# Kernel tuning notes

Hardware: AMD Instinct MI355X
Metric: run time of the kernel (lower is better)

The kernel has to match this reference:

```python
import jax, jax.numpy as jnp
import numpy as np

N = 50000
NUM_GRAPHS = 64
EPS = 1e-16  # PyG softmax denominator epsilon


def _gat_conv(x, src, dst, W, a_src, a_dst, b, heads, out_ch):
    n = x.shape[0]
    h = (x @ W).reshape(n, heads, out_ch)                    # [N,H,C]
    al_s = jnp.einsum('nhc,hc->nh', h, a_src)                # [N,H]
    al_d = jnp.einsum('nhc,hc->nh', h, a_dst)                # [N,H]
    e = jax.nn.leaky_relu(al_s[src] + al_d[dst], 0.2)        # [E,H]
    emax = jax.ops.segment_max(e, dst, num_segments=n)       # [N,H]
    ee = jnp.exp(e - emax[dst])
    den = jax.ops.segment_sum(ee, dst, num_segments=n)       # [N,H]
    alpha = ee / (den[dst] + EPS)                            # [E,H]
    msg = h[src] * alpha[:, :, None]                         # [E,H,C]
    out = jax.ops.segment_sum(msg, dst, num_segments=n)      # [N,H,C]
    return out.reshape(n, heads * out_ch) + b


def setup_inputs() -> dict:
    key = jax.random.key(0)
    ks = jax.random.split(key, 16)
    E = 250000
    x = jax.random.normal(ks[0], (N, 11), dtype=jnp.float32)
    edge_index = jax.random.randint(ks[1], (2, E), 0, N, dtype=jnp.int64)
    batch = jnp.sort(jax.random.randint(ks[2], (N,), 0, NUM_GRAPHS, dtype=jnp.int64))
    def glorot(k, shape):
        fan = shape[0] + shape[-1]
        return jax.random.uniform(k, shape, jnp.float32, -1.0, 1.0) * np.sqrt(6.0 / fan)
    return {
        'x': x, 'edge_index': edge_index, 'batch': batch,
        'W1': glorot(ks[3], (11, 8 * 128)),
        'a1s': glorot(ks[4], (8, 128)), 'a1d': glorot(ks[5], (8, 128)),
        'b1': jnp.zeros((8 * 128,), jnp.float32),
        'W2': glorot(ks[6], (1024, 8 * 64)),
        'a2s': glorot(ks[7], (8, 64)), 'a2d': glorot(ks[8], (8, 64)),
        'b2': jnp.zeros((8 * 64,), jnp.float32),
        'W3': glorot(ks[9], (512, 4 * 32)),
        'a3s': glorot(ks[10], (4, 32)), 'a3d': glorot(ks[11], (4, 32)),
        'b3': jnp.zeros((4 * 32,), jnp.float32),
        'Wout': glorot(ks[12], (128, 1)),
        'bout': jnp.zeros((1,), jnp.float32),
    }


def reference(x, edge_index, batch, W1, a1s, a1d, b1, W2, a2s, a2d, b2,
              W3, a3s, a3d, b3, Wout, bout):
    n = x.shape[0]
    # GATConv adds self-loops by default
    loop = jnp.arange(n, dtype=edge_index.dtype)
    src = jnp.concatenate([edge_index[0], loop])
    dst = jnp.concatenate([edge_index[1], loop])
    h = jax.nn.leaky_relu(_gat_conv(x, src, dst, W1, a1s, a1d, b1, 8, 128), 0.01)
    h = jax.nn.leaky_relu(_gat_conv(h, src, dst, W2, a2s, a2d, b2, 8, 64), 0.01)
    h = jax.nn.leaky_relu(_gat_conv(h, src, dst, W3, a3s, a3d, b3, 4, 32), 0.01)
    # global mean pool over graphs
    sums = jax.ops.segment_sum(h, batch, num_segments=NUM_GRAPHS)      # [G,128]
    cnt = jax.ops.segment_sum(jnp.ones((n,), h.dtype), batch, num_segments=NUM_GRAPHS)
    pooled = sums / jnp.maximum(cnt, 1.0)[:, None]
    return pooled @ Wout + bout                                        # [G,1]
```

## Files before the change

kernel.cpp:

```cpp
#include <hip/hip_runtime.h>

#define EPS 1e-16f

typedef __attribute__((ext_vector_type(8))) short short8;
typedef __attribute__((ext_vector_type(4))) float f32x4;

__device__ __forceinline__ float b2f(unsigned short u) {
    return __uint_as_float(((unsigned)u) << 16);
}
__device__ __forceinline__ unsigned short f2b(float f) {
    unsigned u = __float_as_uint(f);
    u += 0x7fffu + ((u >> 16) & 1u);
    return (unsigned short)(u >> 16);
}

typedef __attribute__((address_space(3))) void lds_vp;
typedef __attribute__((address_space(1))) const void glb_vp;
__device__ __forceinline__ void load_lds16(const unsigned short* g,
                                           unsigned short* l) {
    __builtin_amdgcn_global_load_lds((glb_vp*)g, (lds_vp*)l, 16, 0, 0);
}

__global__ void init_deg_kernel(int* deg, int N) {
    int i = blockIdx.x * blockDim.x + threadIdx.x;
    if (i < N) deg[i] = 1;
}

__global__ void hist_kernel(const int* __restrict__ ei, int E, int N, int* deg) {
    int e = blockIdx.x * blockDim.x + threadIdx.x;
    if (e < E) {
        int d = ei[E + e];
        if ((unsigned)d < (unsigned)N) atomicAdd(&deg[d], 1);
    }
}

__global__ void scan_block_kernel(const int* __restrict__ deg,
                                  int* __restrict__ rowst,
                                  int* __restrict__ bsum, int N) {
    __shared__ int s[256];
    int t = threadIdx.x, b = blockIdx.x;
    int i = b * 256 + t;
    s[t] = (i < N) ? deg[i] : 0;
    __syncthreads();
    for (int o = 1; o < 256; o <<= 1) {
        int a = (t >= o) ? s[t - o] : 0;
        __syncthreads();
        s[t] += a;
        __syncthreads();
    }
    if (i < N) rowst[i + 1] = s[t];
    if (t == 255) bsum[b] = s[255];
}

__global__ void scan_top_kernel(const int* __restrict__ bsum,
                                int* __restrict__ boff, int NB) {
    __shared__ int psum[65];
    int t = threadIdx.x;
    int chunk = (NB + 63) / 64;
    int lo = t * chunk, hi = lo + chunk;
    if (lo > NB) lo = NB;
    if (hi > NB) hi = NB;
    int s = 0;
    for (int i = lo; i < hi; i++) s += bsum[i];
    psum[t + 1] = s;
    __syncthreads();
    if (t == 0) {
        psum[0] = 0;
        for (int i = 1; i <= 64; i++) psum[i] += psum[i - 1];
    }
    __syncthreads();
    int run = psum[t];
    for (int i = lo; i < hi; i++) {
        boff[i] = run;
        run += bsum[i];
    }
}

__global__ void scan_add_kernel(int* __restrict__ rowst,
                                const int* __restrict__ boff, int N) {
    int i = blockIdx.x * 256 + threadIdx.x;
    if (i == 0) rowst[0] = 0;
    if (i < N) rowst[i + 1] += boff[blockIdx.x];
}

__global__ void selfloop_kernel(const int* __restrict__ rowst, int* srcs,
                                int* cursor, int N) {
    int n = blockIdx.x * blockDim.x + threadIdx.x;
    if (n < N) {
        srcs[rowst[n]] = n;
        cursor[n] = rowst[n] + 1;
    }
}

__global__ void scatter_kernel(const int* __restrict__ ei, int E, int N,
                               int* cursor, int* srcs) {
    int e = blockIdx.x * blockDim.x + threadIdx.x;
    if (e < E) {
        int d = ei[E + e];
        if ((unsigned)d < (unsigned)N) {
            int p = atomicAdd(&cursor[d], 1);
            int s = ei[e];
            if ((unsigned)s >= (unsigned)N) s = d;
            srcs[p] = s;
        }
    }
}

__global__ void wa1_kernel(const float* __restrict__ W1,
                           const float* __restrict__ a1s,
                           const float* __restrict__ a1d,
                           float* __restrict__ w_as, float* __restrict__ w_ad) {
    int t = threadIdx.x;
    if (t >= 88) return;
    int h = t / 11, k = t % 11;
    float s = 0.f, d = 0.f;
    for (int c = 0; c < 128; c++) {
        float w = W1[k * 1024 + h * 128 + c];
        s += w * a1s[h * 128 + c];
        d += w * a1d[h * 128 + c];
    }
    w_as[h * 16 + k] = s;
    w_ad[h * 16 + k] = d;
}

__global__ void al1_kernel(const float* __restrict__ x,
                           const float* __restrict__ w_as,
                           const float* __restrict__ w_ad,
                           float* __restrict__ als, float* __restrict__ ald,
                           int N) {
    int i = blockIdx.x * blockDim.x + threadIdx.x;
    if (i >= N * 8) return;
    int n = i >> 3, h = i & 7;
    float s = 0.f, d = 0.f;
#pragma unroll
    for (int k = 0; k < 11; k++) {
        float xv = x[n * 11 + k];
        s += xv * w_as[h * 16 + k];
        d += xv * w_ad[h * 16 + k];
    }
    als[i] = s;
    ald[i] = d;
}

__global__ void aggx_kernel(const float* __restrict__ x,
                            const float* __restrict__ escr,
                            const int* __restrict__ rowst,
                            const int* __restrict__ srcs,
                            unsigned short* __restrict__ A2, int N) {
    int n = blockIdx.x;
    int t = threadIdx.x;
    int h = t >> 4, k = t & 15;
    int start = rowst[n], end = rowst[n + 1];
    float acc = 0.f;
    const int CH = 4;
    for (int idx = start; idx < end; idx += CH) {
        int mc = end - idx;
        if (mc > CH) mc = CH;
        int ss[CH];
        float av[CH], xv[CH];
#pragma unroll
        for (int j = 0; j < CH; j++)
            if (j < mc) ss[j] = srcs[idx + j];
#pragma unroll
        for (int j = 0; j < CH; j++)
            if (j < mc) av[j] = escr[(size_t)(idx + j) * 8 + h];
#pragma unroll
        for (int j = 0; j < CH; j++)
            if (j < mc) xv[j] = (k < 11) ? x[ss[j] * 11 + k] : 0.f;
#pragma unroll
        for (int j = 0; j < CH; j++)
            if (j < mc) acc += av[j] * xv[j];
    }
    A2[(size_t)n * 128 + t] = f2b(acc);
}

__global__ void w1bd_kernel(const float* __restrict__ W1,
                            unsigned short* __restrict__ Bt) {
    int i = blockIdx.x * blockDim.x + threadIdx.x;
    if (i >= 1024 * 128) return;
    int n = i >> 7, kk = i & 127;
    int h = kk >> 4, k = kk & 15;
    float v = (h == (n >> 7) && k < 11) ? W1[k * 1024 + n] : 0.f;
    Bt[i] = f2b(v);
}

__global__ void transpose_w_kernel(const float* __restrict__ W,
                                   unsigned short* __restrict__ Wt, int K, int N) {
    int i = blockIdx.x * blockDim.x + threadIdx.x;
    if (i >= K * N) return;
    int k = i / N, n = i % N;
    Wt[(size_t)n * K + k] = f2b(W[i]);
}

template <bool EPI, int HB, int CC>
__global__ __launch_bounds__(256) void gemm_mfma(
    const unsigned short* __restrict__ A, const unsigned short* __restrict__ Bt,
    unsigned short* __restrict__ C, const float* __restrict__ bias,
    const float* __restrict__ a_s, const float* __restrict__ a_d,
    float* __restrict__ als, float* __restrict__ ald, int H, int M, int N,
    int K) {
    int NX = gridDim.x;
    int bid = blockIdx.y * NX + blockIdx.x;
    int win = bid & (8 * NX - 1);
    int mg = bid / (8 * NX);
    int m_t = mg * 8 + (win & 7);
    int n_t = win >> 3;
    int bm = m_t * 128, bn = n_t * 128;
    if (bm >= M) return;

    union SMem {
        struct {
            unsigned short As[2][128 * 32];
            unsigned short Bs[2][128 * 32];
        } k;
        unsigned short Ct[128 * 132];
    };
    __shared__ __align__(16) SMem sm;
    auto& As = sm.k.As;
    auto& Bs = sm.k.Bs;
    auto& Ct = sm.Ct;

    int t = threadIdx.x;
    int w = t >> 6, lane = t & 63;
    int quad = lane >> 4, l16 = lane & 15;
    int wr = (w >> 1) * 64, wc = (w & 1) * 64;

    int c0 = w * 128 + lane;
    int c1 = c0 + 64;
    int r0 = c0 >> 2, p0 = c0 & 3;
    int r1 = c1 >> 2, p1 = c1 & 3;
    int j0 = (p0 - (r0 >> 1)) & 3;
    int j1 = (p1 - (r1 >> 1)) & 3;
    int ga0 = bm + r0;
    if (ga0 >= M) ga0 = M - 1;
    int ga1 = bm + r1;
    if (ga1 >= M) ga1 = M - 1;
    const unsigned short* Ag0 = A + (size_t)ga0 * K + j0 * 8;
    const unsigned short* Ag1 = A + (size_t)ga1 * K + j1 * 8;
    const unsigned short* Bg0 = Bt + (size_t)(bn + r0) * K + j0 * 8;
    const unsigned short* Bg1 = Bt + (size_t)(bn + r1) * K + j1 * 8;

    auto stage = [&](int st, int k0) {
        load_lds16(Ag0 + k0, &As[st][(w * 128) * 8]);
        load_lds16(Ag1 + k0, &As[st][(w * 128 + 64) * 8]);
        load_lds16(Bg0 + k0, &Bs[st][(w * 128) * 8]);
        load_lds16(Bg1 + k0, &Bs[st][(w * 128 + 64) * 8]);
    };

    int aoff[4], boff4[4];
#pragma unroll
    for (int i = 0; i < 4; i++) {
        int ra = wr + i * 16 + l16;
        aoff[i] = ra * 32 + (((quad + (ra >> 1)) & 3) * 8);
        int rb = wc + i * 16 + l16;
        boff4[i] = rb * 32 + (((quad + (rb >> 1)) & 3) * 8);
    }

    f32x4 acc[4][4] = {};
    stage(0, 0);
    int st = 0;
    for (int k0 = 0; k0 < K; k0 += 32, st ^= 1) {
        __syncthreads();
        if (k0 + 32 < K) stage(st ^ 1, k0 + 32);
        short8 a[4], b[4];
#pragma unroll
        for (int mi = 0; mi < 4; mi++) a[mi] = *(const short8*)&As[st][aoff[mi]];
#pragma unroll
        for (int ni = 0; ni < 4; ni++) b[ni] = *(const short8*)&Bs[st][boff4[ni]];
#pragma unroll
        for (int mi = 0; mi < 4; mi++)
#pragma unroll
            for (int ni = 0; ni < 4; ni++)
                acc[mi][ni] = __builtin_amdgcn_mfma_f32_16x16x32_bf16(
                    a[mi], b[ni], acc[mi][ni], 0, 0, 0);
    }
    __syncthreads();

#pragma unroll
    for (int mi = 0; mi < 4; mi++) {
#pragma unroll
        for (int r = 0; r < 4; r++) {
            int rl = wr + mi * 16 + quad * 4 + r;
#pragma unroll
            for (int ni = 0; ni < 4; ni++) {
                int cl = wc + ni * 16 + l16;
                float v = acc[mi][ni][r];
                if (EPI) {
                    v += bias[bn + cl];
                    v = v > 0.f ? v : 0.01f * v;
                }
                Ct[rl * 132 + cl] = f2b(v);
            }
        }
    }
    __syncthreads();
#pragma unroll
    for (int p = 0; p < 16; p++) {
        int q = p * 256 + t;
        int row = q >> 5, c8 = q & 31;
        if (bm + row < M) {
            uint2 v = *(const uint2*)&Ct[row * 132 + c8 * 4];
            *(uint2*)&C[(size_t)(bm + row) * N + bn + c8 * 4] = v;
        }
    }
    if (HB > 0) {
        for (int pi = t; pi < 128 * HB; pi += 256) {
            int row = pi / HB, hl = pi % HB;
            if (bm + row >= M) continue;
            int hg = bn / CC + hl;
            const unsigned short* rp = &Ct[row * 132 + hl * CC];
            const float* asp = a_s + hg * CC;
            const float* adp = a_d + hg * CC;
            float s = 0.f, d = 0.f;
#pragma unroll
            for (int c = 0; c < CC; c++) {
                float v = b2f(rp[c]);
                s += v * asp[c];
                d += v * adp[c];
            }
            als[(size_t)(bm + row) * H + hg] = s;
            ald[(size_t)(bm + row) * H + hg] = d;
        }
    }
}

template <int H>
__global__ void mden_kernel(const float* __restrict__ als,
                            const float* __restrict__ ald,
                            const int* __restrict__ rowst,
                            const int* __restrict__ srcs,
                            float* __restrict__ escr, int N) {
    int i = blockIdx.x * blockDim.x + threadIdx.x;
    if (i >= N * H) return;
    int n = i / H, h = i % H;
    float aldn = ald[i];
    int start = rowst[n], end = rowst[n + 1];
    const int CH = 4;
    float m = -1e30f;
    for (int idx = start; idx < end; idx += CH) {
        int mc = end - idx;
        if (mc > CH) mc = CH;
        int ss[CH];
        float lv[CH];
#pragma unroll
        for (int j = 0; j < CH; j++)
            if (j < mc) ss[j] = srcs[idx + j];
#pragma unroll
        for (int j = 0; j < CH; j++)
            if (j < mc) lv[j] = als[ss[j] * H + h];
#pragma unroll
        for (int j = 0; j < CH; j++)
            if (j < mc) {
                float v = lv[j] + aldn;
                v = v > 0.f ? v : 0.2f * v;
                m = fmaxf(m, v);
            }
    }
    float den = 0.f;
    for (int idx = start; idx < end; idx += CH) {
        int mc = end - idx;
        if (mc > CH) mc = CH;
        int ss[CH];
        float lv[CH];
#pragma unroll
        for (int j = 0; j < CH; j++)
            if (j < mc) ss[j] = srcs[idx + j];
#pragma unroll
        for (int j = 0; j < CH; j++)
            if (j < mc) lv[j] = als[ss[j] * H + h];
#pragma unroll
        for (int j = 0; j < CH; j++)
            if (j < mc) {
                float v = lv[j] + aldn;
                v = v > 0.f ? v : 0.2f * v;
                den += expf(v - m);
            }
    }
    float dinv = 1.0f / (den + EPS);
    for (int idx = start; idx < end; idx += CH) {
        int mc = end - idx;
        if (mc > CH) mc = CH;
        int ss[CH];
        float lv[CH];
#pragma unroll
        for (int j = 0; j < CH; j++)
            if (j < mc) ss[j] = srcs[idx + j];
#pragma unroll
        for (int j = 0; j < CH; j++)
            if (j < mc) lv[j] = als[ss[j] * H + h];
#pragma unroll
        for (int j = 0; j < CH; j++)
            if (j < mc) {
                float v = lv[j] + aldn;
                v = v > 0.f ? v : 0.2f * v;
                escr[(size_t)(idx + j) * H + h] = expf(v - m) * dinv;
            }
    }
}

template <int H, int C>
__global__ void agg_kernel4(const unsigned short* __restrict__ hin,
                            const float* __restrict__ escr,
                            const int* __restrict__ rowst,
                            const int* __restrict__ srcs,
                            const float* __restrict__ bias,
                            unsigned short* __restrict__ out, int N) {
    constexpr int HC = H * C;
    int n = blockIdx.x;
    int t = threadIdx.x;
    int c = t * 4;
    int hh = c / C;
    int start = rowst[n], end = rowst[n + 1];
    float a0 = 0.f, a1 = 0.f, a2 = 0.f, a3 = 0.f;
    const int CH = 4;
    for (int idx = start; idx < end; idx += CH) {
        int mc = end - idx;
        if (mc > CH) mc = CH;
        int ss[CH];
        float av[CH];
        ushort4 uv[CH];
#pragma unroll
        for (int j = 0; j < CH; j++)
            if (j < mc) ss[j] = srcs[idx + j];
#pragma unroll
        for (int j = 0; j < CH; j++)
            if (j < mc) av[j] = escr[(size_t)(idx + j) * H + hh];
#pragma unroll
        for (int j = 0; j < CH; j++)
            if (j < mc) uv[j] = *(const ushort4*)(hin + (size_t)ss[j] * HC + c);
#pragma unroll
        for (int j = 0; j < CH; j++)
            if (j < mc) {
                a0 += av[j] * b2f(uv[j].x);
                a1 += av[j] * b2f(uv[j].y);
                a2 += av[j] * b2f(uv[j].z);
                a3 += av[j] * b2f(uv[j].w);
            }
    }
    float v0 = a0 + bias[c], v1 = a1 + bias[c + 1];
    float v2 = a2 + bias[c + 2], v3 = a3 + bias[c + 3];
    ushort4 o;
    o.x = f2b(v0 > 0.f ? v0 : 0.01f * v0);
    o.y = f2b(v1 > 0.f ? v1 : 0.01f * v1);
    o.z = f2b(v2 > 0.f ? v2 : 0.01f * v2);
    o.w = f2b(v3 > 0.f ? v3 : 0.01f * v3);
    *(ushort4*)&out[(size_t)n * HC + c] = o;
}

template <int H, int C, int TPB>
__global__ void agg_kernel2(const unsigned short* __restrict__ hin,
                            const float* __restrict__ escr,
                            const int* __restrict__ rowst,
                            const int* __restrict__ srcs,
                            const float* __restrict__ bias,
                            unsigned short* __restrict__ out, int N) {
    constexpr int HC = H * C;
    int n = blockIdx.x;
    int t = threadIdx.x;
    int c = t * 2;
    int hh = c / C;
    int start = rowst[n], end = rowst[n + 1];
    float a0 = 0.f, a1 = 0.f;
    const int CH = 4;
    for (int idx = start; idx < end; idx += CH) {
        int mc = end - idx;
        if (mc > CH) mc = CH;
        int ss[CH];
        float av[CH];
        ushort2 uv[CH];
#pragma unroll
        for (int j = 0; j < CH; j++)
            if (j < mc) ss[j] = srcs[idx + j];
#pragma unroll
        for (int j = 0; j < CH; j++)
            if (j < mc) av[j] = escr[(size_t)(idx + j) * H + hh];
#pragma unroll
        for (int j = 0; j < CH; j++)
            if (j < mc) uv[j] = *(const ushort2*)(hin + (size_t)ss[j] * HC + c);
#pragma unroll
        for (int j = 0; j < CH; j++)
            if (j < mc) {
                a0 += av[j] * b2f(uv[j].x);
                a1 += av[j] * b2f(uv[j].y);
            }
    }
    float v0 = a0 + bias[c], v1 = a1 + bias[c + 1];
    ushort2 o;
    o.x = f2b(v0 > 0.f ? v0 : 0.01f * v0);
    o.y = f2b(v1 > 0.f ? v1 : 0.01f * v1);
    *(ushort2*)&out[(size_t)n * HC + c] = o;
}

__global__ void pool_init_kernel(float* pool, int GC) {
    int i = blockIdx.x * blockDim.x + threadIdx.x;
    if (i < GC) pool[i] = 0.f;
}

__global__ void pool_partial_kernel(const unsigned short* __restrict__ h3,
                                    const int* __restrict__ batch,
                                    float* __restrict__ pool, int N, int G) {
    int lo = blockIdx.x * 128;
    int hi = lo + 128;
    if (hi > N) hi = N;
    if (lo >= N) return;
    int t = threadIdx.x;
    int cur = batch[lo];
    float acc = 0.f;
    for (int n = lo; n < hi; n++) {
        int g = batch[n];
        if (g != cur) {
            if ((unsigned)cur < (unsigned)G) atomicAdd(&pool[cur * 128 + t], acc);
            acc = 0.f;
            cur = g;
        }
        acc += b2f(h3[(size_t)n * 128 + t]);
    }
    if ((unsigned)cur < (unsigned)G) atomicAdd(&pool[cur * 128 + t], acc);
}

__global__ void head_kernel(const float* __restrict__ pool,
                            const int* __restrict__ batch,
                            const float* __restrict__ Wout,
                            const float* __restrict__ bout,
                            float* __restrict__ out, int N) {
    int g = blockIdx.x;
    int t = threadIdx.x;
    int lo, hi;
    {
        int a = 0, b = N;
        while (a < b) { int mid = (a + b) >> 1; if (batch[mid] < g) a = mid + 1; else b = mid; }
        lo = a;
        a = lo; b = N;
        while (a < b) { int mid = (a + b) >> 1; if (batch[mid] < g + 1) a = mid + 1; else b = mid; }
        hi = a;
    }
    float c = (float)(hi - lo);
    c = c > 1.f ? c : 1.f;
    float v = (pool[g * 128 + t] / c) * Wout[t];
    for (int o = 32; o; o >>= 1) v += __shfl_xor(v, o);
    __shared__ float partial[2];
    if ((t & 63) == 0) partial[t >> 6] = v;
    __syncthreads();
    if (t == 0) out[g] = partial[0] + partial[1] + bout[0];
}

extern "C" void kernel_launch(void* const* d_in, const int* in_sizes, int n_in,
                              void* d_out, int out_size, void* d_ws,
                              size_t ws_size, hipStream_t stream) {
    const float* x = (const float*)d_in[0];
    const int* ei = (const int*)d_in[1];
    const int* batch = (const int*)d_in[2];
    const float* W1 = (const float*)d_in[3];
    const float* a1s = (const float*)d_in[4];
    const float* a1d = (const float*)d_in[5];
    const float* b1 = (const float*)d_in[6];
    const float* W2 = (const float*)d_in[7];
    const float* a2s = (const float*)d_in[8];
    const float* a2d = (const float*)d_in[9];
    const float* b2 = (const float*)d_in[10];
    const float* W3 = (const float*)d_in[11];
    const float* a3s = (const float*)d_in[12];
    const float* a3d = (const float*)d_in[13];
    const float* b3 = (const float*)d_in[14];
    const float* Wout = (const float*)d_in[15];
    const float* bout = (const float*)d_in[16];
    float* out = (float*)d_out;

    const int N = in_sizes[0] / 11;
    const int E = in_sizes[1] / 2;
    const int Etot = E + N;
    const int G = out_size;
    const int NB = (N + 255) / 256;
    const int MT = ((N + 127) / 128 + 7) / 8 * 8;

    char* ws = (char*)d_ws;
    size_t off = 0;
    auto alloc = [&](size_t bytes) -> void* {
        void* p = ws + off;
        off += (bytes + 255) & ~(size_t)255;
        return p;
    };
    unsigned short* buf1 = (unsigned short*)alloc((size_t)N * 1024 * 2);
    unsigned short* buf2 = (unsigned short*)alloc((size_t)N * 1024 * 2);
    float* als = (float*)alloc((size_t)N * 8 * 4);
    float* ald = (float*)alloc((size_t)N * 8 * 4);
    float* escr = (float*)alloc((size_t)Etot * 8 * 4);
    int* rowst = (int*)alloc((size_t)(N + 1) * 4);
    int* cursor = (int*)alloc((size_t)N * 4);
    int* srcs = (int*)alloc((size_t)Etot * 4);
    int* deg = (int*)alloc((size_t)N * 4);
    int* bsum = (int*)alloc((size_t)NB * 4);
    int* boff = (int*)alloc((size_t)NB * 4);
    float* pool = (float*)alloc((size_t)G * 128 * 4);
    unsigned short* aggx = (unsigned short*)alloc((size_t)N * 128 * 2);
    unsigned short* w1bd = (unsigned short*)alloc((size_t)1024 * 128 * 2);
    unsigned short* wt2 = (unsigned short*)alloc((size_t)1024 * 512 * 2);
    unsigned short* wt3 = (unsigned short*)alloc((size_t)512 * 128 * 2);
    float* w_as = (float*)alloc(8 * 16 * 4);
    float* w_ad = (float*)alloc(8 * 16 * 4);

    int nb = (N + 255) / 256;
    int eb = (E + 255) / 256;

    init_deg_kernel<<<nb, 256, 0, stream>>>(deg, N);
    hist_kernel<<<eb, 256, 0, stream>>>(ei, E, N, deg);
    scan_block_kernel<<<NB, 256, 0, stream>>>(deg, rowst, bsum, N);
    scan_top_kernel<<<1, 64, 0, stream>>>(bsum, boff, NB);
    scan_add_kernel<<<NB, 256, 0, stream>>>(rowst, boff, N);
    selfloop_kernel<<<nb, 256, 0, stream>>>(rowst, srcs, cursor, N);
    scatter_kernel<<<eb, 256, 0, stream>>>(ei, E, N, cursor, srcs);

    wa1_kernel<<<1, 128, 0, stream>>>(W1, a1s, a1d, w_as, w_ad);
    w1bd_kernel<<<(1024 * 128 + 255) / 256, 256, 0, stream>>>(W1, w1bd);
    transpose_w_kernel<<<(1024 * 512 + 255) / 256, 256, 0, stream>>>(W2, wt2,
                                                                     1024, 512);
    transpose_w_kernel<<<(512 * 128 + 255) / 256, 256, 0, stream>>>(W3, wt3,
                                                                    512, 128);

    al1_kernel<<<(N * 8 + 255) / 256, 256, 0, stream>>>(x, w_as, w_ad, als, ald,
                                                        N);
    mden_kernel<8><<<(N * 8 + 255) / 256, 256, 0, stream>>>(als, ald, rowst,
                                                            srcs, escr, N);
    aggx_kernel<<<N, 128, 0, stream>>>(x, escr, rowst, srcs, aggx, N);
    gemm_mfma<true, 0, 1><<<dim3(8, MT), 256, 0, stream>>>(
        aggx, w1bd, buf2, b1, nullptr, nullptr, nullptr, nullptr, 0, N, 1024,
        128);

    gemm_mfma<false, 2, 64><<<dim3(4, MT), 256, 0, stream>>>(
        buf2, wt2, buf1, nullptr, a2s, a2d, als, ald, 8, N, 512, 1024);
    mden_kernel<8><<<(N * 8 + 255) / 256, 256, 0, stream>>>(als, ald, rowst,
                                                            srcs, escr, N);
    agg_kernel4<8, 64><<<N, 128, 0, stream>>>(buf1, escr, rowst, srcs, b2, buf2,
                                              N);

    gemm_mfma<false, 4, 32><<<dim3(1, MT), 256, 0, stream>>>(
        buf2, wt3, buf1, nullptr, a3s, a3d, als, ald, 4, N, 128, 512);
    mden_kernel<4><<<(N * 4 + 255) / 256, 256, 0, stream>>>(als, ald, rowst,
                                                            srcs, escr, N);
    agg_kernel2<4, 32, 64><<<N, 64, 0, stream>>>(buf1, escr, rowst, srcs, b3,
                                                 buf2, N);

    pool_init_kernel<<<(G * 128 + 255) / 256, 256, 0, stream>>>(pool, G * 128);
    pool_partial_kernel<<<(N + 127) / 128, 128, 0, stream>>>(buf2, batch, pool,
                                                             N, G);
    head_kernel<<<G, 128, 0, stream>>>(pool, batch, Wout, bout, out, N);
}
```

Baseline: 495.1 us.

## Fuse edge softmax into aggregation kernels for layers 2 and 3

```diff
diff --git a/kernel.cpp b/kernel.cpp
--- a/kernel.cpp
+++ b/kernel.cpp
@@ -353,6 +353,7 @@
             if (j < mc) {
                 float v = lv[j] + aldn;
                 v = v > 0.f ? v : 0.2f * v;
+                escr[(size_t)(idx + j) * H + h] = v;
                 m = fmaxf(m, v);
             }
     }
@@ -360,81 +361,91 @@
     for (int idx = start; idx < end; idx += CH) {
         int mc = end - idx;
         if (mc > CH) mc = CH;
-        int ss[CH];
         float lv[CH];
 #pragma unroll
         for (int j = 0; j < CH; j++)
-            if (j < mc) ss[j] = srcs[idx + j];
-#pragma unroll
-        for (int j = 0; j < CH; j++)
-            if (j < mc) lv[j] = als[ss[j] * H + h];
-#pragma unroll
-        for (int j = 0; j < CH; j++)
-            if (j < mc) {
-                float v = lv[j] + aldn;
-                v = v > 0.f ? v : 0.2f * v;
-                den += expf(v - m);
-            }
+            if (j < mc) lv[j] = escr[(size_t)(idx + j) * H + h];
+#pragma unroll
+        for (int j = 0; j < CH; j++)
+            if (j < mc) den += expf(lv[j] - m);
     }
     float dinv = 1.0f / (den + EPS);
     for (int idx = start; idx < end; idx += CH) {
         int mc = end - idx;
         if (mc > CH) mc = CH;
-        int ss[CH];
         float lv[CH];
 #pragma unroll
         for (int j = 0; j < CH; j++)
-            if (j < mc) ss[j] = srcs[idx + j];
-#pragma unroll
-        for (int j = 0; j < CH; j++)
-            if (j < mc) lv[j] = als[ss[j] * H + h];
-#pragma unroll
-        for (int j = 0; j < CH; j++)
-            if (j < mc) {
-                float v = lv[j] + aldn;
-                v = v > 0.f ? v : 0.2f * v;
-                escr[(size_t)(idx + j) * H + h] = expf(v - m) * dinv;
-            }
+            if (j < mc) lv[j] = escr[(size_t)(idx + j) * H + h];
+#pragma unroll
+        for (int j = 0; j < CH; j++)
+            if (j < mc)
+                escr[(size_t)(idx + j) * H + h] = expf(lv[j] - m) * dinv;
     }
 }
 
 template <int H, int C>
-__global__ void agg_kernel4(const unsigned short* __restrict__ hin,
-                            const float* __restrict__ escr,
-                            const int* __restrict__ rowst,
-                            const int* __restrict__ srcs,
-                            const float* __restrict__ bias,
-                            unsigned short* __restrict__ out, int N) {
+__global__ void agg_fused4(const unsigned short* __restrict__ hin,
+                           const float* __restrict__ als,
+                           const float* __restrict__ ald,
+                           const int* __restrict__ rowst,
+                           const int* __restrict__ srcs,
+                           const float* __restrict__ bias,
+                           unsigned short* __restrict__ out, int N) {
     constexpr int HC = H * C;
+    constexpr int TPH = C / 4;
     int n = blockIdx.x;
     int t = threadIdx.x;
     int c = t * 4;
     int hh = c / C;
+    int li = (c % C) / 4;
     int start = rowst[n], end = rowst[n + 1];
+    float aldn = ald[n * H + hh];
+    float m = -1e30f;
+    for (int idx = start + li; idx < end; idx += TPH) {
+        float v = als[srcs[idx] * H + hh] + aldn;
+        v = v > 0.f ? v : 0.2f * v;
+        m = fmaxf(m, v);
+    }
+#pragma unroll
+    for (int o = 1; o < TPH; o <<= 1) m = fmaxf(m, __shfl_xor(m, o));
+    float den = 0.f;
+    for (int idx = start + li; idx < end; idx += TPH) {
+        float v = als[srcs[idx] * H + hh] + aldn;
+        v = v > 0.f ? v : 0.2f * v;
+        den += expf(v - m);
+    }
+#pragma unroll
+    for (int o = 1; o < TPH; o <<= 1) den += __shfl_xor(den, o);
+    float dinv = 1.0f / (den + EPS);
+
     float a0 = 0.f, a1 = 0.f, a2 = 0.f, a3 = 0.f;
     const int CH = 4;
     for (int idx = start; idx < end; idx += CH) {
         int mc = end - idx;
         if (mc > CH) mc = CH;
         int ss[CH];
-        float av[CH];
+        float lv[CH];
         ushort4 uv[CH];
 #pragma unroll
         for (int j = 0; j < CH; j++)
             if (j < mc) ss[j] = srcs[idx + j];
 #pragma unroll
         for (int j = 0; j < CH; j++)
-            if (j < mc) av[j] = escr[(size_t)(idx + j) * H + hh];
+            if (j < mc) lv[j] = als[ss[j] * H + hh];
 #pragma unroll
         for (int j = 0; j < CH; j++)
             if (j < mc) uv[j] = *(const ushort4*)(hin + (size_t)ss[j] * HC + c);
 #pragma unroll
         for (int j = 0; j < CH; j++)
             if (j < mc) {
-                a0 += av[j] * b2f(uv[j].x);
-                a1 += av[j] * b2f(uv[j].y);
-                a2 += av[j] * b2f(uv[j].z);
-                a3 += av[j] * b2f(uv[j].w);
+                float v = lv[j] + aldn;
+                v = v > 0.f ? v : 0.2f * v;
+                float a = expf(v - m) * dinv;
+                a0 += a * b2f(uv[j].x);
+                a1 += a * b2f(uv[j].y);
+                a2 += a * b2f(uv[j].z);
+                a3 += a * b2f(uv[j].w);
             }
     }
     float v0 = a0 + bias[c], v1 = a1 + bias[c + 1];
@@ -447,41 +458,66 @@
     *(ushort4*)&out[(size_t)n * HC + c] = o;
 }
 
-template <int H, int C, int TPB>
-__global__ void agg_kernel2(const unsigned short* __restrict__ hin,
-                            const float* __restrict__ escr,
-                            const int* __restrict__ rowst,
-                            const int* __restrict__ srcs,
-                            const float* __restrict__ bias,
-                            unsigned short* __restrict__ out, int N) {
+template <int H, int C>
+__global__ void agg_fused2(const unsigned short* __restrict__ hin,
+                           const float* __restrict__ als,
+                           const float* __restrict__ ald,
+                           const int* __restrict__ rowst,
+                           const int* __restrict__ srcs,
+                           const float* __restrict__ bias,
+                           unsigned short* __restrict__ out, int N) {
     constexpr int HC = H * C;
+    constexpr int TPH = C / 2;
     int n = blockIdx.x;
     int t = threadIdx.x;
     int c = t * 2;
     int hh = c / C;
+    int li = (c % C) / 2;
     int start = rowst[n], end = rowst[n + 1];
+    float aldn = ald[n * H + hh];
+    float m = -1e30f;
+    for (int idx = start + li; idx < end; idx += TPH) {
+        float v = als[srcs[idx] * H + hh] + aldn;
+        v = v > 0.f ? v : 0.2f * v;
+        m = fmaxf(m, v);
+    }
+#pragma unroll
+    for (int o = 1; o < TPH; o <<= 1) m = fmaxf(m, __shfl_xor(m, o));
+    float den = 0.f;
+    for (int idx = start + li; idx < end; idx += TPH) {
+        float v = als[srcs[idx] * H + hh] + aldn;
+        v = v > 0.f ? v : 0.2f * v;
+        den += expf(v - m);
+    }
+#pragma unroll
+    for (int o = 1; o < TPH; o <<= 1) den += __shfl_xor(den, o);
+    float dinv = 1.0f / (den + EPS);
+
     float a0 = 0.f, a1 = 0.f;
     const int CH = 4;
     for (int idx = start; idx < end; idx += CH) {
         int mc = end - idx;
         if (mc > CH) mc = CH;
         int ss[CH];
-        float av[CH];
+        float lv[CH];
         ushort2 uv[CH];
 #pragma unroll
         for (int j = 0; j < CH; j++)
             if (j < mc) ss[j] = srcs[idx + j];
 #pragma unroll
         for (int j = 0; j < CH; j++)
-            if (j < mc) av[j] = escr[(size_t)(idx + j) * H + hh];
+            if (j < mc) lv[j] = als[ss[j] * H + hh];
 #pragma unroll
         for (int j = 0; j < CH; j++)
             if (j < mc) uv[j] = *(const ushort2*)(hin + (size_t)ss[j] * HC + c);
 #pragma unroll
         for (int j = 0; j < CH; j++)
             if (j < mc) {
-                a0 += av[j] * b2f(uv[j].x);
-                a1 += av[j] * b2f(uv[j].y);
+                float v = lv[j] + aldn;
+                v = v > 0.f ? v : 0.2f * v;
+                float a = expf(v - m) * dinv;
+                a0 += a * b2f(uv[j].x);
+                a1 += a * b2f(uv[j].y);
             }
     }
     float v0 = a0 + bias[c], v1 = a1 + bias[c + 1];
@@ -628,17 +664,13 @@
 
     gemm_mfma<false, 2, 64><<<dim3(4, MT), 256, 0, stream>>>(
         buf2, wt2, buf1, nullptr, a2s, a2d, als, ald, 8, N, 512, 1024);
-    mden_kernel<8><<<(N * 8 + 255) / 256, 256, 0, stream>>>(als, ald, rowst,
-                                                            srcs, escr, N);
-    agg_kernel4<8, 64><<<N, 128, 0, stream>>>(buf1, escr, rowst, srcs, b2, buf2,
-                                              N);
+    agg_fused4<8, 64><<<N, 128, 0, stream>>>(buf1, als, ald, rowst, srcs, b2,
+                                             buf2, N);
 
     gemm_mfma<false, 4, 32><<<dim3(1, MT), 256, 0, stream>>>(
         buf2, wt3, buf1, nullptr, a3s, a3d, als, ald, 4, N, 128, 512);
-    mden_kernel<4><<<(N * 4 + 255) / 256, 256, 0, stream>>>(als, ald, rowst,
-                                                            srcs, escr, N);
-    agg_kernel2<4, 32, 64><<<N, 64, 0, stream>>>(buf1, escr, rowst, srcs, b3,
-                                                 buf2, N);
+    agg_fused2<4, 32><<<N, 64, 0, stream>>>(buf1, als, ald, rowst, srcs, b3,
+                                            buf2, N);
 
     pool_init_kernel<<<(G * 128 + 255) / 256, 256, 0, stream>>>(pool, G * 128);
     pool_partial_kernel<<<(N + 127) / 128, 128, 0, stream>>>(buf2, batch, pool,
```

After: 491.6 us. Within noise of the previous version (-0.7%).
